# Kernel tuning notes

Hardware: AMD Instinct MI355X
Metric: run time of the kernel (lower is better)

## Reference

```python
import jax, jax.numpy as jnp
import numpy as np

B, S, UNITS = 32, 2048, 512
D = 2 * UNITS  # 1024


def setup_inputs() -> dict:
    key = jax.random.key(0)
    ks = jax.random.split(key, 12)
    s = 1.0 / np.sqrt(D)
    mask = (jax.random.uniform(ks[0], (B, S)) < 0.9).astype(jnp.float32)
    mask = mask.at[:, 0].set(1.0)  # guarantee no all-zero row
    return {
        "dec_hidden": jax.random.normal(ks[1], (2, B, UNITS), dtype=jnp.float32),
        "enc_output": jax.random.normal(ks[2], (B, S, D), dtype=jnp.float32),
        "enc_pad_mask": mask,
        "prev_coverage": jax.random.uniform(ks[3], (B, S), dtype=jnp.float32) * 0.1,
        "Wh": jax.random.uniform(ks[4], (D, D), minval=-s, maxval=s),
        "bh": jax.random.uniform(ks[5], (D,), minval=-s, maxval=s),
        "Ws": jax.random.uniform(ks[6], (D, D), minval=-s, maxval=s),
        "bs": jax.random.uniform(ks[7], (D,), minval=-s, maxval=s),
        "Wc": jax.random.uniform(ks[8], (D, 1), minval=-1.0, maxval=1.0),
        "bc": jax.random.uniform(ks[9], (D,), minval=-1.0, maxval=1.0),
        "v": jax.random.uniform(ks[10], (1, D), minval=-s, maxval=s),
        "bv": jax.random.uniform(ks[11], (1,), minval=-s, maxval=s),
        "use_coverage": 1,
    }


def reference(dec_hidden, enc_output, enc_pad_mask, prev_coverage,
              Wh, bh, Ws, bs, Wc, bc, v, bv, use_coverage):
    # dec_hidden: (2, B, units) -> (B, 1, 2*units)
    dec = jnp.transpose(dec_hidden, (1, 0, 2)).reshape(dec_hidden.shape[1], 1, -1)
    enc_features = jnp.einsum('bsd,ed->bse', enc_output, Wh) + bh  # (B,S,D)
    dec_features = jnp.einsum('bod,ed->boe', dec, Ws) + bs          # (B,1,D)
    att_inputs = enc_features + dec_features
    if use_coverage:
        # Linear(1 -> D) applied to prev_coverage[..., None]
        coverage_features = prev_coverage[:, :, None] * Wc[:, 0][None, None, :] + bc
        att_inputs = att_inputs + coverage_features
    score = jnp.einsum('bsd,od->bso', jnp.tanh(att_inputs), v) + bv  # (B,S,1)
    attention_weights = jax.nn.softmax(score, axis=1)[..., 0]        # (B,S)
    attention_weights = attention_weights * enc_pad_mask
    attention_weights = attention_weights / jnp.sum(attention_weights, axis=1, keepdims=True)
    context_vector = jnp.einsum('bs,bsd->bd', attention_weights, enc_output)
    if use_coverage:
        coverage_vector = prev_coverage + attention_weights
        return context_vector, attention_weights, coverage_vector
    return context_vector, attention_weights
```

## Files before the change

kernel.cpp:

```cpp
#include <hip/hip_runtime.h>
#include <hip/hip_bf16.h>

#define BATCH 32
#define SEQ   2048
#define DIM   1024

typedef __attribute__((ext_vector_type(4))) float f32x4;
typedef __attribute__((ext_vector_type(8))) short short8;
typedef __attribute__((ext_vector_type(4))) ushort u16x4;

static __device__ __forceinline__ ushort f2bf(float x) {
    __hip_bfloat16 h = __float2bfloat16(x);
    union { __hip_bfloat16 h; ushort u; } cv; cv.h = h;
    return cv.u;
}

static __device__ __forceinline__ void gll16(const void* g, void* l) {
    __builtin_amdgcn_global_load_lds(
        (const __attribute__((address_space(1))) void*)g,
        (__attribute__((address_space(3))) void*)l, 16, 0, 0);
}

__global__ __launch_bounds__(256) void kWhPack(const float* __restrict__ Wh,
                                               ushort* __restrict__ whbp) {
    int g = blockIdx.x * 256 + threadIdx.x;
    int l  = g & 63;
    int kb = (g >> 6) & 31;
    int eb = g >> 11;
    int e  = eb * 16 + (l & 15);
    int k0 = kb * 32 + (l >> 4) * 8;
    const float* src = Wh + (size_t)e * DIM + k0;
    float4 a = *(const float4*)src;
    float4 b = *(const float4*)(src + 4);
    union { ushort us[8]; uint4 u4; } pk;
    pk.us[0] = f2bf(a.x); pk.us[1] = f2bf(a.y); pk.us[2] = f2bf(a.z); pk.us[3] = f2bf(a.w);
    pk.us[4] = f2bf(b.x); pk.us[5] = f2bf(b.y); pk.us[6] = f2bf(b.z); pk.us[7] = f2bf(b.w);
    *(uint4*)(whbp + (size_t)g * 8) = pk.u4;
}

__global__ __launch_bounds__(256) void kBase(const float* __restrict__ dh,
                                             const float* __restrict__ Ws,
                                             const float* __restrict__ bs,
                                             const float* __restrict__ bh,
                                             const float* __restrict__ bc,
                                             const int* __restrict__ uc,
                                             float* __restrict__ base) {
    __shared__ float dec[8][DIM];
    int ec = blockIdx.x >> 2;
    int bg = blockIdx.x & 3;
    int b0 = bg * 8, e0 = ec * 32;
    int tid = threadIdx.x;
    for (int i = tid; i < 8 * DIM; i += 256) {
        int bb = i >> 10, d = i & 1023;
        float vdec = (d < 512) ? dh[(b0 + bb) * 512 + d]
                               : dh[BATCH * 512 + (b0 + bb) * 512 + d - 512];
        dec[bb][d] = vdec;
    }
    __syncthreads();
    int el = tid >> 3, ds = tid & 7;
    int e = e0 + el;
    float acc[8] = {0.f, 0.f, 0.f, 0.f, 0.f, 0.f, 0.f, 0.f};
    const float* wrow = Ws + (size_t)e * DIM;
    for (int i = 0; i < 128; ++i) {
        int d = i * 8 + ds;
        float wv = wrow[d];
#pragma unroll
        for (int bb = 0; bb < 8; ++bb) acc[bb] += wv * dec[bb][d];
    }
#pragma unroll
    for (int bb = 0; bb < 8; ++bb) {
        float s = acc[bb];
        s += __shfl_xor(s, 1); s += __shfl_xor(s, 2); s += __shfl_xor(s, 4);
        acc[bb] = s;
    }
    if (ds == 0) {
        float bias = bs[e] + bh[e] + ((*uc) ? bc[e] : 0.0f);
#pragma unroll
        for (int bb = 0; bb < 8; ++bb) base[(b0 + bb) * DIM + e] = acc[bb] + bias;
    }
}

__global__ __launch_bounds__(1024, 4) void kScore(const float* __restrict__ enc,
                                                  const ushort* __restrict__ whbp,
                                                  const float* __restrict__ base,
                                                  const float* __restrict__ pc,
                                                  const float* __restrict__ Wc,
                                                  const float* __restrict__ vv,
                                                  const int* __restrict__ uc,
                                                  float* __restrict__ scorep) {
    __shared__ ushort Bl[2][16384];
    __shared__ ushort Al[2][128 * 40];
    __shared__ float pcl[128];
    __shared__ float red[16][64];

    const int tid = threadIdx.x;
    const int w = tid >> 6;
    const int lane = tid & 63;
    const int q = lane >> 4, l15 = lane & 15;
    const int wm = w >> 3, wn = w & 7;

    const int hb = blockIdx.x;
    const int nq = (hb >> 3) & 1;
    const int rg = ((hb >> 4) << 3) + (hb & 7);
    const int b = rg >> 4;
    const int s0 = (rg & 15) << 7;

    const float* Ab = enc + ((size_t)(b * SEQ + s0)) * DIM;
    if (tid < 128) pcl[tid] = pc[b * SEQ + s0 + tid];

    const int arow = tid >> 3, ak4 = (tid & 7) << 2;
    const float* agsrc = Ab + (size_t)arow * DIM + ak4;
    const int awidx = arow * 40 + ak4;

    const int ebg0 = nq * 32 + w * 2;
    const ushort* bgsrc0 = whbp + ((size_t)(ebg0 + 0) << 14) + (lane << 3);
    const ushort* bgsrc1 = whbp + ((size_t)(ebg0 + 1) << 14) + (lane << 3);
    ushort* bdst0_base0 = &Bl[0][(w * 2 + 0) * 512];
    ushort* bdst1_base0 = &Bl[0][(w * 2 + 1) * 512];

    f32x4 acc[4][4] = {};

    {
        gll16(bgsrc0, bdst0_base0);
        gll16(bgsrc1, bdst1_base0);
        float4 a4 = *(const float4*)agsrc;
        u16x4 p; p[0] = f2bf(a4.x); p[1] = f2bf(a4.y); p[2] = f2bf(a4.z); p[3] = f2bf(a4.w);
        *(u16x4*)&Al[0][awidx] = p;
    }
    __syncthreads();

    int buf = 0;
    for (int kt = 0; kt < 32; ++kt) {
        float4 a4;
        if (kt < 31) {
            gll16(bgsrc0 + ((size_t)(kt + 1) << 9), &Bl[buf ^ 1][(w * 2 + 0) * 512]);
            gll16(bgsrc1 + ((size_t)(kt + 1) << 9), &Bl[buf ^ 1][(w * 2 + 1) * 512]);
            a4 = *(const float4*)(agsrc + (kt + 1) * 32);
        }
        short8 af[4], bf[4];
#pragma unroll
        for (int mf = 0; mf < 4; ++mf)
            af[mf] = *(const short8*)&Al[buf][(wm * 64 + mf * 16 + l15) * 40 + q * 8];
#pragma unroll
        for (int ef = 0; ef < 4; ++ef)
            bf[ef] = *(const short8*)&Bl[buf][(wn * 4 + ef) * 512 + lane * 8];
#pragma unroll
        for (int ef = 0; ef < 4; ++ef)
#pragma unroll
            for (int mf = 0; mf < 4; ++mf)
                acc[mf][ef] = __builtin_amdgcn_mfma_f32_16x16x32_bf16(af[mf], bf[ef], acc[mf][ef], 0, 0, 0);
        if (kt < 31) {
            u16x4 p; p[0] = f2bf(a4.x); p[1] = f2bf(a4.y); p[2] = f2bf(a4.z); p[3] = f2bf(a4.w);
            *(u16x4*)&Al[buf ^ 1][awidx] = p;
        }
        __syncthreads();
        buf ^= 1;
    }

    const float ucf = (float)(*uc);
    float basee[4], ve[4], wce[4];
#pragma unroll
    for (int ef = 0; ef < 4; ++ef) {
        int e = nq * 512 + wn * 64 + ef * 16 + l15;
        basee[ef] = base[b * DIM + e];
        ve[ef] = vv[e];
        wce[ef] = Wc[e] * ucf;
    }
#pragma unroll
    for (int mf = 0; mf < 4; ++mf) {
#pragma unroll
        for (int r = 0; r < 4; ++r) {
            int rl = (mf << 4) + (q << 2) + r;
            float p = pcl[wm * 64 + rl];
            float sp = 0.f;
#pragma unroll
            for (int ef = 0; ef < 4; ++ef) {
                float x = acc[mf][ef][r] + basee[ef] + p * wce[ef];
                float t = 1.0f - 2.0f / (1.0f + __expf(2.0f * x));
                sp += t * ve[ef];
            }
            sp += __shfl_xor(sp, 1);
            sp += __shfl_xor(sp, 2);
            sp += __shfl_xor(sp, 4);
            sp += __shfl_xor(sp, 8);
            if (l15 == 0) red[w][rl] = sp;
        }
    }
    __syncthreads();
    if (tid < 128) {
        int wmf = tid >> 6, rl = tid & 63;
        float s = 0.f;
#pragma unroll
        for (int j = 0; j < 8; ++j) s += red[wmf * 8 + j][rl];
        scorep[nq * (BATCH * SEQ) + b * SEQ + s0 + tid] = s;
    }
}

__global__ __launch_bounds__(512) void kSoftmax(const float* __restrict__ scorep,
                                                const float* __restrict__ mask,
                                                const float* __restrict__ pc,
                                                float* __restrict__ att,
                                                float* __restrict__ cov,
                                                int write_cov) {
    __shared__ float rmax[8], rsum[8];
    int b = blockIdx.x, tid = threadIdx.x;
    int wv = tid >> 6, ln = tid & 63;
    float x[4];
#pragma unroll
    for (int i = 0; i < 4; ++i) {
        int idx = b * SEQ + tid + i * 512;
        x[i] = scorep[idx] + scorep[BATCH * SEQ + idx];
    }
    float m = fmaxf(fmaxf(x[0], x[1]), fmaxf(x[2], x[3]));
#pragma unroll
    for (int o = 1; o < 64; o <<= 1) m = fmaxf(m, __shfl_xor(m, o));
    if (ln == 0) rmax[wv] = m;
    __syncthreads();
    m = rmax[0];
#pragma unroll
    for (int i = 1; i < 8; ++i) m = fmaxf(m, rmax[i]);

    float ms[4], wm[4];
#pragma unroll
    for (int i = 0; i < 4; ++i) ms[i] = mask[b * SEQ + tid + i * 512];
    float s = 0.f;
#pragma unroll
    for (int i = 0; i < 4; ++i) { wm[i] = __expf(x[i] - m) * ms[i]; s += wm[i]; }
#pragma unroll
    for (int o = 1; o < 64; o <<= 1) s += __shfl_xor(s, o);
    if (ln == 0) rsum[wv] = s;
    __syncthreads();
    s = 0.f;
#pragma unroll
    for (int i = 0; i < 8; ++i) s += rsum[i];
    float inv = 1.0f / s;
#pragma unroll
    for (int i = 0; i < 4; ++i) {
        float wf = wm[i] * inv;
        att[b * SEQ + tid + i * 512] = wf;
        if (write_cov) cov[b * SEQ + tid + i * 512] = pc[b * SEQ + tid + i * 512] + wf;
    }
}

__global__ __launch_bounds__(256) void kCtxPart(const float* __restrict__ enc,
                                                const float* __restrict__ att,
                                                float* __restrict__ part) {
    __shared__ float wl[64];
    int bx = blockIdx.x;
    int b = bx >> 5, sc = bx & 31;
    int tid = threadIdx.x;
    if (tid < 64) wl[tid] = att[b * SEQ + sc * 64 + tid];
    __syncthreads();
    const float* basep = enc + ((size_t)(b * SEQ + sc * 64)) * DIM + tid * 4;
    float4 acc = {0.f, 0.f, 0.f, 0.f};
#pragma unroll 4
    for (int i = 0; i < 64; ++i) {
        float w = wl[i];
        float4 xv = *(const float4*)(basep + (size_t)i * DIM);
        acc.x += w * xv.x; acc.y += w * xv.y; acc.z += w * xv.z; acc.w += w * xv.w;
    }
    *(float4*)(part + (size_t)bx * DIM + tid * 4) = acc;
}

__global__ __launch_bounds__(256) void kCtxReduce(const float* __restrict__ part,
                                                  float* __restrict__ ctx) {
    int g = blockIdx.x * 256 + threadIdx.x;
    int b = g >> 10, d = g & 1023;
    float s = 0.f;
#pragma unroll
    for (int i = 0; i < 32; ++i) s += part[((size_t)(b * 32 + i) << 10) + d];
    ctx[g] = s;
}

extern "C" void kernel_launch(void* const* d_in, const int* in_sizes, int n_in,
                              void* d_out, int out_size, void* d_ws, size_t ws_size,
                              hipStream_t stream) {
    const float* dh   = (const float*)d_in[0];
    const float* enc  = (const float*)d_in[1];
    const float* mask = (const float*)d_in[2];
    const float* pc   = (const float*)d_in[3];
    const float* Wh   = (const float*)d_in[4];
    const float* bh   = (const float*)d_in[5];
    const float* Ws   = (const float*)d_in[6];
    const float* bs   = (const float*)d_in[7];
    const float* Wc   = (const float*)d_in[8];
    const float* bc   = (const float*)d_in[9];
    const float* vv   = (const float*)d_in[10];
    const int* uc     = (const int*)d_in[12];

    float* ctx = (float*)d_out;
    float* att = ctx + BATCH * DIM;
    float* cov = att + BATCH * SEQ;
    int write_cov = (out_size >= BATCH * (DIM + 2 * SEQ)) ? 1 : 0;

    ushort* whbp  = (ushort*)d_ws;
    float* base   = (float*)((char*)d_ws + 2u * 1024u * 1024u);
    float* scorep = base + BATCH * DIM;
    float* part   = scorep + 2 * BATCH * SEQ;

    kWhPack<<<512, 256, 0, stream>>>(Wh, whbp);
    kBase<<<128, 256, 0, stream>>>(dh, Ws, bs, bh, bc, uc, base);
    kScore<<<1024, 1024, 0, stream>>>(enc, whbp, base, pc, Wc, vv, uc, scorep);
    kSoftmax<<<BATCH, 512, 0, stream>>>(scorep, mask, pc, att, cov, write_cov);
    kCtxPart<<<1024, 256, 0, stream>>>(enc, att, part);
    kCtxReduce<<<128, 256, 0, stream>>>(part, ctx);
}
```

Before: 270.5 us.

## Retile score GEMM into small blocks reading packed Wh directly from global

The score GEMM moves from 1024-thread blocks with 128x512 tiles, where packed Wh is staged through LDS via global_load_lds, to 256-thread blocks with 64x256 tiles. B fragments are now loaded straight from global/L2 into registers, and only the activation tile goes through LDS with a 64-wide k step. This frees a large amount of LDS and allows more, smaller blocks, but each block now re-reads A from HBM for four column quarters and issues uncached per-wave B loads. The score partials grow from two to four slices, and the softmax kernel sums all four.

```diff
diff --git a/kernel.cpp b/kernel.cpp
--- a/kernel.cpp
+++ b/kernel.cpp
@@ -7,18 +7,11 @@
 
 typedef __attribute__((ext_vector_type(4))) float f32x4;
 typedef __attribute__((ext_vector_type(8))) short short8;
-typedef __attribute__((ext_vector_type(4))) ushort u16x4;
 
 static __device__ __forceinline__ ushort f2bf(float x) {
     __hip_bfloat16 h = __float2bfloat16(x);
     union { __hip_bfloat16 h; ushort u; } cv; cv.h = h;
     return cv.u;
-}
-
-static __device__ __forceinline__ void gll16(const void* g, void* l) {
-    __builtin_amdgcn_global_load_lds(
-        (const __attribute__((address_space(1))) void*)g,
-        (__attribute__((address_space(3))) void*)l, 16, 0, 0);
 }
 
 __global__ __launch_bounds__(256) void kWhPack(const float* __restrict__ Wh,
@@ -80,78 +73,87 @@
     }
 }
 
-__global__ __launch_bounds__(1024, 4) void kScore(const float* __restrict__ enc,
-                                                  const ushort* __restrict__ whbp,
-                                                  const float* __restrict__ base,
-                                                  const float* __restrict__ pc,
-                                                  const float* __restrict__ Wc,
-                                                  const float* __restrict__ vv,
-                                                  const int* __restrict__ uc,
-                                                  float* __restrict__ scorep) {
-    __shared__ ushort Bl[2][16384];
-    __shared__ ushort Al[2][128 * 40];
-    __shared__ float pcl[128];
-    __shared__ float red[16][64];
+__global__ __launch_bounds__(256, 4) void kScore(const float* __restrict__ enc,
+                                                 const ushort* __restrict__ whbp,
+                                                 const float* __restrict__ base,
+                                                 const float* __restrict__ pc,
+                                                 const float* __restrict__ Wc,
+                                                 const float* __restrict__ vv,
+                                                 const int* __restrict__ uc,
+                                                 float* __restrict__ scorep) {
+    __shared__ ushort Al[2][64 * 72];
+    __shared__ float pcl[64];
+    __shared__ float red[4][64];
 
     const int tid = threadIdx.x;
     const int w = tid >> 6;
     const int lane = tid & 63;
     const int q = lane >> 4, l15 = lane & 15;
-    const int wm = w >> 3, wn = w & 7;
-
-    const int hb = blockIdx.x;
-    const int nq = (hb >> 3) & 1;
-    const int rg = ((hb >> 4) << 3) + (hb & 7);
-    const int b = rg >> 4;
-    const int s0 = (rg & 15) << 7;
+
+    const int c = blockIdx.x & 7;
+    const int j = blockIdx.x >> 3;
+    const int strip = c * 128 + (j >> 2);
+    const int nq = j & 3;
+    const int b = strip >> 5;
+    const int s0 = (strip & 31) << 6;
 
     const float* Ab = enc + ((size_t)(b * SEQ + s0)) * DIM;
-    if (tid < 128) pcl[tid] = pc[b * SEQ + s0 + tid];
-
-    const int arow = tid >> 3, ak4 = (tid & 7) << 2;
-    const float* agsrc = Ab + (size_t)arow * DIM + ak4;
-    const int awidx = arow * 40 + ak4;
-
-    const int ebg0 = nq * 32 + w * 2;
-    const ushort* bgsrc0 = whbp + ((size_t)(ebg0 + 0) << 14) + (lane << 3);
-    const ushort* bgsrc1 = whbp + ((size_t)(ebg0 + 1) << 14) + (lane << 3);
-    ushort* bdst0_base0 = &Bl[0][(w * 2 + 0) * 512];
-    ushort* bdst1_base0 = &Bl[0][(w * 2 + 1) * 512];
+    if (tid < 64) pcl[tid] = pc[b * SEQ + s0 + tid];
+
+    const int r = tid & 63, kc = tid >> 6;
+    const float* agp = Ab + (size_t)r * DIM + (kc << 4);
+    const int awoff = r * 72 + (kc << 4);
+
+    const ushort* bgp = whbp + ((size_t)((nq << 4) + (w << 2)) << 14) + (lane << 3);
 
     f32x4 acc[4][4] = {};
 
     {
-        gll16(bgsrc0, bdst0_base0);
-        gll16(bgsrc1, bdst1_base0);
-        float4 a4 = *(const float4*)agsrc;
-        u16x4 p; p[0] = f2bf(a4.x); p[1] = f2bf(a4.y); p[2] = f2bf(a4.z); p[3] = f2bf(a4.w);
-        *(u16x4*)&Al[0][awidx] = p;
+        float4 v0 = *(const float4*)agp;
+        float4 v1 = *(const float4*)(agp + 4);
+        float4 v2 = *(const float4*)(agp + 8);
+        float4 v3 = *(const float4*)(agp + 12);
+        union { ushort us[8]; uint4 u4; } p0, p1;
+        p0.us[0] = f2bf(v0.x); p0.us[1] = f2bf(v0.y); p0.us[2] = f2bf(v0.z); p0.us[3] = f2bf(v0.w);
+        p0.us[4] = f2bf(v1.x); p0.us[5] = f2bf(v1.y); p0.us[6] = f2bf(v1.z); p0.us[7] = f2bf(v1.w);
+        p1.us[0] = f2bf(v2.x); p1.us[1] = f2bf(v2.y); p1.us[2] = f2bf(v2.z); p1.us[3] = f2bf(v2.w);
+        p1.us[4] = f2bf(v3.x); p1.us[5] = f2bf(v3.y); p1.us[6] = f2bf(v3.z); p1.us[7] = f2bf(v3.w);
+        *(uint4*)&Al[0][awoff] = p0.u4;
+        *(uint4*)&Al[0][awoff + 8] = p1.u4;
     }
     __syncthreads();
 
     int buf = 0;
-    for (int kt = 0; kt < 32; ++kt) {
-        float4 a4;
-        if (kt < 31) {
-            gll16(bgsrc0 + ((size_t)(kt + 1) << 9), &Bl[buf ^ 1][(w * 2 + 0) * 512]);
-            gll16(bgsrc1 + ((size_t)(kt + 1) << 9), &Bl[buf ^ 1][(w * 2 + 1) * 512]);
-            a4 = *(const float4*)(agsrc + (kt + 1) * 32);
+    for (int kt = 0; kt < 16; ++kt) {
+        float4 v0, v1, v2, v3;
+        if (kt < 15) {
+            const float* p = agp + (kt + 1) * 64;
+            v0 = *(const float4*)p;       v1 = *(const float4*)(p + 4);
+            v2 = *(const float4*)(p + 8); v3 = *(const float4*)(p + 12);
         }
-        short8 af[4], bf[4];
-#pragma unroll
-        for (int mf = 0; mf < 4; ++mf)
-            af[mf] = *(const short8*)&Al[buf][(wm * 64 + mf * 16 + l15) * 40 + q * 8];
-#pragma unroll
-        for (int ef = 0; ef < 4; ++ef)
-            bf[ef] = *(const short8*)&Bl[buf][(wn * 4 + ef) * 512 + lane * 8];
-#pragma unroll
-        for (int ef = 0; ef < 4; ++ef)
+#pragma unroll
+        for (int kb = 0; kb < 2; ++kb) {
+            short8 bf[4], af[4];
+#pragma unroll
+            for (int ef = 0; ef < 4; ++ef)
+                bf[ef] = *(const short8*)(bgp + ((size_t)ef << 14) + ((size_t)((kt << 1) + kb) << 9));
 #pragma unroll
             for (int mf = 0; mf < 4; ++mf)
-                acc[mf][ef] = __builtin_amdgcn_mfma_f32_16x16x32_bf16(af[mf], bf[ef], acc[mf][ef], 0, 0, 0);
-        if (kt < 31) {
-            u16x4 p; p[0] = f2bf(a4.x); p[1] = f2bf(a4.y); p[2] = f2bf(a4.z); p[3] = f2bf(a4.w);
-            *(u16x4*)&Al[buf ^ 1][awidx] = p;
+                af[mf] = *(const short8*)&Al[buf][((mf << 4) + l15) * 72 + (kb << 5) + (q << 3)];
+#pragma unroll
+            for (int ef = 0; ef < 4; ++ef)
+#pragma unroll
+                for (int mf = 0; mf < 4; ++mf)
+                    acc[mf][ef] = __builtin_amdgcn_mfma_f32_16x16x32_bf16(af[mf], bf[ef], acc[mf][ef], 0, 0, 0);
+        }
+        if (kt < 15) {
+            union { ushort us[8]; uint4 u4; } p0, p1;
+            p0.us[0] = f2bf(v0.x); p0.us[1] = f2bf(v0.y); p0.us[2] = f2bf(v0.z); p0.us[3] = f2bf(v0.w);
+            p0.us[4] = f2bf(v1.x); p0.us[5] = f2bf(v1.y); p0.us[6] = f2bf(v1.z); p0.us[7] = f2bf(v1.w);
+            p1.us[0] = f2bf(v2.x); p1.us[1] = f2bf(v2.y); p1.us[2] = f2bf(v2.z); p1.us[3] = f2bf(v2.w);
+            p1.us[4] = f2bf(v3.x); p1.us[5] = f2bf(v3.y); p1.us[6] = f2bf(v3.z); p1.us[7] = f2bf(v3.w);
+            *(uint4*)&Al[buf ^ 1][awoff] = p0.u4;
+            *(uint4*)&Al[buf ^ 1][awoff + 8] = p1.u4;
         }
         __syncthreads();
         buf ^= 1;
@@ -161,7 +163,7 @@
     float basee[4], ve[4], wce[4];
 #pragma unroll
     for (int ef = 0; ef < 4; ++ef) {
-        int e = nq * 512 + wn * 64 + ef * 16 + l15;
+        int e = (nq << 8) + (w << 6) + (ef << 4) + l15;
         basee[ef] = base[b * DIM + e];
         ve[ef] = vv[e];
         wce[ef] = Wc[e] * ucf;
@@ -169,13 +171,13 @@
 #pragma unroll
     for (int mf = 0; mf < 4; ++mf) {
 #pragma unroll
-        for (int r = 0; r < 4; ++r) {
-            int rl = (mf << 4) + (q << 2) + r;
-            float p = pcl[wm * 64 + rl];
+        for (int rr = 0; rr < 4; ++rr) {
+            int rl = (mf << 4) + (q << 2) + rr;
+            float p = pcl[rl];
             float sp = 0.f;
 #pragma unroll
             for (int ef = 0; ef < 4; ++ef) {
-                float x = acc[mf][ef][r] + basee[ef] + p * wce[ef];
+                float x = acc[mf][ef][rr] + basee[ef] + p * wce[ef];
                 float t = 1.0f - 2.0f / (1.0f + __expf(2.0f * x));
                 sp += t * ve[ef];
             }
@@ -187,11 +189,8 @@
         }
     }
     __syncthreads();
-    if (tid < 128) {
-        int wmf = tid >> 6, rl = tid & 63;
-        float s = 0.f;
-#pragma unroll
-        for (int j = 0; j < 8; ++j) s += red[wmf * 8 + j][rl];
+    if (tid < 64) {
+        float s = red[0][tid] + red[1][tid] + red[2][tid] + red[3][tid];
         scorep[nq * (BATCH * SEQ) + b * SEQ + s0 + tid] = s;
     }
 }
@@ -203,13 +202,14 @@
                                                 float* __restrict__ cov,
                                                 int write_cov) {
     __shared__ float rmax[8], rsum[8];
+    const int BS = BATCH * SEQ;
     int b = blockIdx.x, tid = threadIdx.x;
     int wv = tid >> 6, ln = tid & 63;
     float x[4];
 #pragma unroll
     for (int i = 0; i < 4; ++i) {
         int idx = b * SEQ + tid + i * 512;
-        x[i] = scorep[idx] + scorep[BATCH * SEQ + idx];
+        x[i] = (scorep[idx] + scorep[BS + idx]) + (scorep[2 * BS + idx] + scorep[3 * BS + idx]);
     }
     float m = fmaxf(fmaxf(x[0], x[1]), fmaxf(x[2], x[3]));
 #pragma unroll
@@ -296,11 +296,11 @@
     ushort* whbp  = (ushort*)d_ws;
     float* base   = (float*)((char*)d_ws + 2u * 1024u * 1024u);
     float* scorep = base + BATCH * DIM;
-    float* part   = scorep + 2 * BATCH * SEQ;
+    float* part   = scorep + 4 * BATCH * SEQ;
 
     kWhPack<<<512, 256, 0, stream>>>(Wh, whbp);
     kBase<<<128, 256, 0, stream>>>(dh, Ws, bs, bh, bc, uc, base);
-    kScore<<<1024, 1024, 0, stream>>>(enc, whbp, base, pc, Wc, vv, uc, scorep);
+    kScore<<<4096, 256, 0, stream>>>(enc, whbp, base, pc, Wc, vv, uc, scorep);
     kSoftmax<<<BATCH, 512, 0, stream>>>(scorep, mask, pc, att, cov, write_cov);
     kCtxPart<<<1024, 256, 0, stream>>>(enc, att, part);
     kCtxReduce<<<128, 256, 0, stream>>>(part, ctx);
```

Measured after the change: 298.7 us. +10.4%, slower.
